# Kernel tuning notes

Measured on AMD Instinct MI355X. Metric: run time of the kernel, lower is better.

Reference implementation:

```python
import jax, jax.numpy as jnp
import numpy as np

DIM = 768
HEADS = 12
HEAD_DIM = DIM // HEADS
WS = 14  # window size
MLP = 3072
EPS = 1e-6
SCALE = HEAD_DIM ** -0.5
B, H, W = 4, 64, 64


def setup_inputs() -> dict:
    key = jax.random.key(0)
    ks = jax.random.split(key, 8)
    s = 0.02
    f32 = jnp.float32
    return {
        "hidden_states": jax.random.normal(ks[0], (B, DIM, H, W), f32),
        "ln1_w": jnp.ones((DIM,), f32),
        "ln1_b": jnp.zeros((DIM,), f32),
        "qkv_w": jax.random.normal(ks[1], (DIM, 3 * DIM), f32) * s,
        "qkv_b": jnp.zeros((3 * DIM,), f32),
        "proj_w": jax.random.normal(ks[2], (DIM, DIM), f32) * s,
        "proj_b": jnp.zeros((DIM,), f32),
        "rel_pos_h": jax.random.normal(ks[3], (2 * WS - 1, HEAD_DIM), f32) * s,
        "rel_pos_w": jax.random.normal(ks[4], (2 * WS - 1, HEAD_DIM), f32) * s,
        "ln2_w": jnp.ones((DIM,), f32),
        "ln2_b": jnp.zeros((DIM,), f32),
        "fc1_w": jax.random.normal(ks[5], (DIM, MLP), f32) * s,
        "fc1_b": jnp.zeros((MLP,), f32),
        "fc2_w": jax.random.normal(ks[6], (MLP, DIM), f32) * s,
        "fc2_b": jnp.zeros((DIM,), f32),
    }


def _layer_norm(x, w, b):
    mu = jnp.mean(x, axis=-1, keepdims=True)
    var = jnp.mean(jnp.square(x - mu), axis=-1, keepdims=True)
    return (x - mu) * jax.lax.rsqrt(var + EPS) * w + b


def _get_rel_pos(size, rel_pos):
    # q_size == k_size == WS, rel_pos already has 2*WS-1 rows -> pure gather
    coords = jnp.arange(size)[:, None] - jnp.arange(size)[None, :] + (size - 1)
    return rel_pos[coords]  # (size, size, head_dim)


def _attention(x, qkv_w, qkv_b, proj_w, proj_b, rel_pos_h, rel_pos_w):
    nb, h, w, c = x.shape  # windows batch, WS, WS, DIM
    n = h * w
    qkv = x.reshape(nb, n, c) @ qkv_w + qkv_b  # (nb, n, 3*DIM)
    qkv = qkv.reshape(nb, n, 3, HEADS, HEAD_DIM).transpose(2, 0, 3, 1, 4)
    qkv = qkv.reshape(3, nb * HEADS, n, HEAD_DIM)
    q, k, v = qkv[0], qkv[1], qkv[2]
    attn = jnp.einsum('bqc,bkc->bqk', q * SCALE, k)  # (nb*HEADS, n, n)
    # decomposed relative position bias
    Rh = _get_rel_pos(h, rel_pos_h)  # (h, h, hd)
    Rw = _get_rel_pos(w, rel_pos_w)  # (w, w, hd)
    rq = q.reshape(-1, h, w, HEAD_DIM)
    rel_h = jnp.einsum('bhwc,hkc->bhwk', rq, Rh)
    rel_w = jnp.einsum('bhwc,wkc->bhwk', rq, Rw)
    attn = (attn.reshape(-1, h, w, h, w)
            + rel_h[:, :, :, :, None]
            + rel_w[:, :, :, None, :]).reshape(-1, n, n)
    attn = jax.nn.softmax(attn, axis=-1)
    out = attn @ v  # (nb*HEADS, n, hd)
    out = out.reshape(nb, HEADS, h, w, HEAD_DIM).transpose(0, 2, 3, 1, 4)
    out = out.reshape(nb, h, w, c)
    return out @ proj_w + proj_b


def reference(hidden_states, ln1_w, ln1_b, qkv_w, qkv_b, proj_w, proj_b,
              rel_pos_h, rel_pos_w, ln2_w, ln2_b, fc1_w, fc1_b, fc2_w, fc2_b):
    x = hidden_states.transpose(0, 2, 3, 1)  # NCHW -> NHWC
    b, h, w, c = x.shape
    shortcut = x
    x = _layer_norm(x, ln1_w, ln1_b)
    # window partition with padding
    ph = (WS - h % WS) % WS
    pw = (WS - w % WS) % WS
    x = jnp.pad(x, ((0, 0), (0, ph), (0, pw), (0, 0)))
    hp, wp = h + ph, w + pw
    x = x.reshape(b, hp // WS, WS, wp // WS, WS, c).transpose(0, 1, 3, 2, 4, 5)
    windows = x.reshape(-1, WS, WS, c)
    windows = _attention(windows, qkv_w, qkv_b, proj_w, proj_b, rel_pos_h, rel_pos_w)
    # window unpartition + crop
    x = windows.reshape(b, hp // WS, wp // WS, WS, WS, c).transpose(0, 1, 3, 2, 4, 5)
    x = x.reshape(b, hp, wp, c)[:, :h, :w, :]
    x = shortcut + x
    y = _layer_norm(x, ln2_w, ln2_b)
    y = jax.nn.gelu(y @ fc1_w + fc1_b, approximate=False) @ fc2_w + fc2_b
    x = x + y
    return x.transpose(0, 3, 1, 2)  # back to NCHW
```

## Files before the change

### kernel.cpp

```cpp
#include <hip/hip_runtime.h>
#include <cstdint>
#include <cstddef>

#define NIMG   4
#define GRIDSZ 64
#define CH     768
#define NHEAD  12
#define WSZ    14
#define NWINS  100
#define NTOK   196
#define MWIN   19600
#define MREAL  16384
#define MLPC   3072
#define QKSCALE 0.125f

#define KSTR 72
#define VSTR 216
#define PSTR 40

typedef unsigned short u16;
typedef __attribute__((ext_vector_type(8))) short bf16x8;
typedef __attribute__((ext_vector_type(4))) float f32x4;

__device__ __forceinline__ float b2f(u16 u) {
  uint32_t x = (uint32_t)u << 16; float f; __builtin_memcpy(&f, &x, 4); return f;
}
__device__ __forceinline__ u16 f2b(float f) {
  uint32_t x; __builtin_memcpy(&x, &f, 4);
  x += 0x7fffu + ((x >> 16) & 1u);
  return (u16)(x >> 16);
}

__device__ __forceinline__ float fast_gelu(float x) {
  float z  = x * 0.70710678118654752440f;
  float az = fabsf(z);
  float t  = 1.0f / (1.0f + 0.3275911f * az);
  float poly = ((((1.061405429f * t - 1.453152027f) * t + 1.421413741f) * t
                 - 0.284496736f) * t + 0.254829592f) * t;
  float e  = __expf(-az * az);
  float erfv = copysignf(1.0f - poly * e, z);
  return 0.5f * x * (1.0f + erfv);
}

__device__ __forceinline__ void gl_lds16(const u16* g, u16* l) {
  __builtin_amdgcn_global_load_lds(
      (const __attribute__((address_space(1))) unsigned int*)g,
      (__attribute__((address_space(3))) unsigned int*)l, 16, 0, 0);
}

__global__ __launch_bounds__(256) void k_nchw2nhwc(const float* __restrict__ in,
                                                   float* __restrict__ out) {
  __shared__ float tile[32][33];
  int b  = blockIdx.z;
  int g0 = blockIdx.x * 32;
  int c0 = blockIdx.y * 32;
  int tx = threadIdx.x, ty = threadIdx.y;
  const float* ip = in + (size_t)b * CH * 4096;
  float* op = out + (size_t)b * 4096 * CH;
#pragma unroll
  for (int k = 0; k < 32; k += 8)
    tile[ty + k][tx] = ip[(size_t)(c0 + ty + k) * 4096 + g0 + tx];
  __syncthreads();
#pragma unroll
  for (int k = 0; k < 32; k += 8)
    op[(size_t)(g0 + ty + k) * CH + c0 + tx] = tile[tx][ty + k];
}

__global__ __launch_bounds__(256) void k_nhwc2nchw(const float* __restrict__ in,
                                                   float* __restrict__ out) {
  __shared__ float tile[32][33];
  int b  = blockIdx.z;
  int g0 = blockIdx.x * 32;
  int c0 = blockIdx.y * 32;
  int tx = threadIdx.x, ty = threadIdx.y;
  const float* ip = in + (size_t)b * 4096 * CH;
  float* op = out + (size_t)b * CH * 4096;
#pragma unroll
  for (int k = 0; k < 32; k += 8)
    tile[ty + k][tx] = ip[(size_t)(g0 + ty + k) * CH + c0 + tx];
  __syncthreads();
#pragma unroll
  for (int k = 0; k < 32; k += 8)
    op[(size_t)(c0 + ty + k) * 4096 + g0 + tx] = tile[tx][ty + k];
}

__global__ __launch_bounds__(256) void k_wt(const float* __restrict__ in,
                                            u16* __restrict__ out,
                                            int K, int N) {
  __shared__ float t[32][33];
  int n0 = blockIdx.x * 32, k0 = blockIdx.y * 32;
  int tx = threadIdx.x, ty = threadIdx.y;
#pragma unroll
  for (int k = 0; k < 32; k += 8)
    t[ty + k][tx] = in[(size_t)(k0 + ty + k) * N + n0 + tx];
  __syncthreads();
#pragma unroll
  for (int k = 0; k < 32; k += 8)
    out[(size_t)(n0 + ty + k) * K + k0 + tx] = f2b(t[tx][ty + k]);
}

__device__ __forceinline__ float block_sum(float s, float* red) {
  __syncthreads();
#pragma unroll
  for (int off = 32; off > 0; off >>= 1) s += __shfl_down(s, off, 64);
  int wid = threadIdx.x >> 6, lane = threadIdx.x & 63;
  if (lane == 0) red[wid] = s;
  __syncthreads();
  return red[0] + red[1] + red[2] + red[3];
}

__global__ __launch_bounds__(256) void k_ln(const float* __restrict__ x,
                                            const float* __restrict__ wt,
                                            const float* __restrict__ bs,
                                            u16* __restrict__ y,
                                            int window_mode) {
  __shared__ float red[4];
  int row = blockIdx.x, tid = threadIdx.x;
  const float* xp = x + (size_t)row * CH;
  float v0 = xp[tid], v1 = xp[tid + 256], v2 = xp[tid + 512];
  float mu = block_sum(v0 + v1 + v2, red) * (1.0f / 768.0f);
  float d0 = v0 - mu, d1 = v1 - mu, d2 = v2 - mu;
  float var = block_sum(d0 * d0 + d1 * d1 + d2 * d2, red) * (1.0f / 768.0f);
  float rs = rsqrtf(var + 1e-6f);
  int orow = row;
  if (window_mode) {
    int b = row >> 12, hw = row & 4095;
    int h = hw >> 6, wc = hw & 63;
    orow = (b * 25 + (h / WSZ) * 5 + (wc / WSZ)) * NTOK + (h % WSZ) * WSZ + (wc % WSZ);
  }
  u16* yp = y + (size_t)orow * CH;
  yp[tid]       = f2b(d0 * rs * wt[tid]       + bs[tid]);
  yp[tid + 256] = f2b(d1 * rs * wt[tid + 256] + bs[tid + 256]);
  yp[tid + 512] = f2b(d2 * rs * wt[tid + 512] + bs[tid + 512]);
}

__global__ __launch_bounds__(256, 3) void k_gemm_mfma(const u16* __restrict__ A,
                                                      const u16* __restrict__ BT,
                                                      const float* __restrict__ bias,
                                                      void* __restrict__ Cv,
                                                      u16* __restrict__ Vt,
                                                      int M, int N, int K,
                                                      int act, int mode, int row0) {
  __shared__ u16 As[3][128 * 32];
  __shared__ u16 Bs[3][128 * 32];
  int tid  = threadIdx.x;
  int lane = tid & 63, wave = tid >> 6;

  int gx   = gridDim.x, gy = gridDim.y;
  int nwg  = gx * gy;
  int orig = blockIdx.y * gx + blockIdx.x;
  int q = nwg >> 3, r = nwg & 7;
  int xcd = orig & 7, idx = orig >> 3;
  int wgid = (xcd < r ? xcd * (q + 1) : r * (q + 1) + (xcd - r) * q) + idx;

  int GM = 3145728 / (128 * K * 2);
  if (GM < 2) GM = 2;
  if (GM > gy) GM = gy;
  int gsz   = GM * gx;
  int grp   = wgid / gsz;
  int first = grp * GM;
  int gm    = gy - first; if (gm > GM) gm = GM;
  int loc   = wgid - grp * gsz;
  int bm    = first + loc % gm;
  int bn    = loc / gm;

  int wm = (wave & 1) * 64, wn = (wave >> 1) * 64;
  int l15 = lane & 15, quad = lane >> 4;
  int xq = (quad ^ ((l15 >> 1) & 3)) * 8;

  f32x4 acc[4][4];
#pragma unroll
  for (int i = 0; i < 4; i++)
#pragma unroll
    for (int j = 0; j < 4; j++) acc[i][j] = (f32x4){0.f, 0.f, 0.f, 0.f};

  const u16* Atile = A + (size_t)bm * 128 * K;
  const u16* Btile = BT + (size_t)bn * 128 * K;

  const u16* ga[2];
  const u16* gb[2];
#pragma unroll
  for (int i = 0; i < 2; ++i) {
    int c_ = i * 256 + wave * 64 + lane;
    int row_ = c_ >> 2, gs_ = (c_ & 3) ^ ((c_ >> 3) & 3);
    ga[i] = Atile + (size_t)row_ * K + gs_ * 8;
    gb[i] = Btile + (size_t)row_ * K + gs_ * 8;
  }

  const int nk = K >> 5;

#define STAGE(slot)                                                          \
  do {                                                                       \
    _Pragma("unroll")                                                        \
    for (int i = 0; i < 2; ++i) {                                            \
      gl_lds16(ga[i], &As[(slot)][(i * 256 + wave * 64) * 8]);               \
      ga[i] += 32;                                                           \
      gl_lds16(gb[i], &Bs[(slot)][(i * 256 + wave * 64) * 8]);               \
      gb[i] += 32;                                                           \
    }                                                                        \
  } while (0)

#define COMPUTE(slot)                                                        \
  do {                                                                       \
    bf16x8 af[4], bfv[4];                                                    \
    _Pragma("unroll")                                                        \
    for (int mi = 0; mi < 4; mi++)                                           \
      af[mi] = *(const bf16x8*)&As[(slot)][(wm + mi * 16 + l15) * 32 + xq];  \
    _Pragma("unroll")                                                        \
    for (int ni = 0; ni < 4; ni++)                                           \
      bfv[ni] = *(const bf16x8*)&Bs[(slot)][(wn + ni * 16 + l15) * 32 + xq]; \
    _Pragma("unroll")                                                        \
    for (int mi = 0; mi < 4; mi++)                                           \
      _Pragma("unroll")                                                      \
      for (int ni = 0; ni < 4; ni++)                                         \
        acc[mi][ni] = __builtin_amdgcn_mfma_f32_16x16x32_bf16(               \
            bfv[ni], af[mi], acc[mi][ni], 0, 0, 0);                          \
  } while (0)

#define WAITL                                                                \
  do {                                                                       \
    asm volatile("s_waitcnt vmcnt(4)" ::: "memory");                         \
    __builtin_amdgcn_s_barrier();                                            \
  } while (0)

  STAGE(0);
  STAGE(1);

  for (int g = 0; g < nk - 3; g += 3) {
    WAITL; STAGE(2); COMPUTE(0);
    WAITL; STAGE(0); COMPUTE(1);
    WAITL; STAGE(1); COMPUTE(2);
  }
  WAITL; STAGE(2); COMPUTE(0);
  WAITL;           COMPUTE(1);
  asm volatile("s_waitcnt vmcnt(0)" ::: "memory");
  __builtin_amdgcn_s_barrier();
  COMPUTE(2);

#undef STAGE
#undef COMPUTE
#undef WAITL

#pragma unroll
  for (int mi = 0; mi < 4; mi++) {
    int row = bm * 128 + wm + mi * 16 + l15;
    if (row >= M) continue;
    size_t gbase = 0;
    bool valid = true;
    int wloc = 0, tok = 0;
    if (mode == 2) {
      int rowa = row + row0;
      int widx = rowa / NTOK, tt = rowa % NTOK;
      int b = widx / 25, wq = widx % 25;
      int h = (wq / 5) * WSZ + tt / WSZ;
      int w = (wq % 5) * WSZ + tt % WSZ;
      valid = (h < GRIDSZ) && (w < GRIDSZ);
      gbase = valid ? ((size_t)((b * GRIDSZ + h) * GRIDSZ + w)) * CH : 0;
    }
    if (mode == 3) { wloc = row / NTOK; tok = row - wloc * NTOK; }
#pragma unroll
    for (int ni = 0; ni < 4; ni++) {
      int colb = bn * 128 + wn + ni * 16 + quad * 4;
      float4 b4 = *(const float4*)&bias[colb];
      float v[4] = {acc[mi][ni][0] + b4.x, acc[mi][ni][1] + b4.y,
                    acc[mi][ni][2] + b4.z, acc[mi][ni][3] + b4.w};
      if (act == 1) {
#pragma unroll
        for (int r2 = 0; r2 < 4; r2++) v[r2] = fast_gelu(v[r2]);
      }
      if (mode == 0) {
        ushort4 st = make_ushort4(f2b(v[0]), f2b(v[1]), f2b(v[2]), f2b(v[3]));
        *(ushort4*)((u16*)Cv + (size_t)row * N + colb) = st;
      } else if (mode == 1) {
        float4* p = (float4*)((float*)Cv + (size_t)row * N + colb);
        float4 o = *p;
        o.x += v[0]; o.y += v[1]; o.z += v[2]; o.w += v[3];
        *p = o;
      } else if (mode == 2) {
        if (valid) {
          float4* p = (float4*)((float*)Cv + gbase + colb);
          float4 o = *p;
          o.x += v[0]; o.y += v[1]; o.z += v[2]; o.w += v[3];
          *p = o;
        }
      } else {
        if (colb < 1536) {
          ushort4 st = make_ushort4(f2b(v[0]), f2b(v[1]), f2b(v[2]), f2b(v[3]));
          *(ushort4*)((u16*)Cv + (size_t)row * N + colb) = st;
        } else {
          int vv = colb - 1536, hd = vv >> 6, d = vv & 63;
          u16* vp = Vt + ((size_t)(wloc * NHEAD + hd) * 64 + d) * VSTR + tok;
#pragma unroll
          for (int r2 = 0; r2 < 4; r2++) vp[(size_t)r2 * VSTR] = f2b(v[r2]);
        }
      }
    }
  }
}

__global__ __launch_bounds__(256) void k_relbias(const u16* __restrict__ qkv,
                                                 const float* __restrict__ rel_h,
                                                 const float* __restrict__ rel_w,
                                                 u16* __restrict__ rhg,
                                                 u16* __restrict__ rwg,
                                                 int nrows) {
  int idx = blockIdx.x * 256 + threadIdx.x;
  if (idx >= nrows * NHEAD) return;
  int head = idx % NHEAD, row = idx / NHEAD;
  int wloc = row / NTOK, tok = row - wloc * NTOK;
  const u16* qp = qkv + (size_t)row * (3 * CH) + head * 64;
  float q[64];
#pragma unroll
  for (int d = 0; d < 64; d += 4) {
    ushort4 u4 = *(const ushort4*)(qp + d);
    q[d] = b2f(u4.x); q[d + 1] = b2f(u4.y); q[d + 2] = b2f(u4.z); q[d + 3] = b2f(u4.w);
  }
  int hq = tok / WSZ, wq = tok % WSZ;
  size_t obase = ((size_t)(wloc * NHEAD + head) * NTOK + tok) * 16;
  for (int kk = 0; kk < WSZ; kk++) {
    const float* rh = rel_h + (size_t)(hq - kk + WSZ - 1) * 64;
    const float* rw = rel_w + (size_t)(wq - kk + WSZ - 1) * 64;
    float sh = 0.0f, sw = 0.0f;
#pragma unroll
    for (int d = 0; d < 64; d++) { sh += q[d] * rh[d]; sw += q[d] * rw[d]; }
    rhg[obase + kk] = f2b(sh);
    rwg[obase + kk] = f2b(sw);
  }
}

__global__ __launch_bounds__(256) void k_attn_mfma(const u16* __restrict__ qkv,
                                                   const u16* __restrict__ Vt,
                                                   const u16* __restrict__ rhg,
                                                   const u16* __restrict__ rwg,
                                                   u16* __restrict__ out,
                                                   int win0) {
  __shared__ u16 Ks[NTOK * KSTR];
  __shared__ u16 Vs[64 * VSTR];
  __shared__ u16 Ps[4][16 * PSTR];
  int head = blockIdx.x, wloc = blockIdx.y;
  int tid = threadIdx.x, lane = tid & 63, wave = tid >> 6;
  int l15 = lane & 15, quad = lane >> 4;
  const u16* qbase = qkv + (size_t)wloc * NTOK * (3 * CH) + head * 64;

  for (int c = tid; c < NTOK * 8; c += 256) {
    int tok = c >> 3, part = c & 7;
    uint4 v = *(const uint4*)(qbase + (size_t)tok * (3 * CH) + CH + part * 8);
    *(uint4*)&Ks[tok * KSTR + part * 8] = v;
  }
  const u16* vb = Vt + (size_t)(wloc * NHEAD + head) * 64 * VSTR;
#pragma unroll
  for (int it = 0; it < 7; ++it) {
    int c = it * 256 + tid;
    if (c < 64 * VSTR / 8) gl_lds16(vb + (size_t)c * 8, Vs + ((size_t)it * 256 + wave * 64) * 8);
  }
  __syncthreads();

  const u16* rhp = rhg + ((size_t)(wloc * NHEAD + head) * NTOK) * 16;
  const u16* rwp = rwg + ((size_t)(wloc * NHEAD + head) * NTOK) * 16;
  int winabs = win0 + wloc;

  for (int t16 = wave; t16 < 13; t16 += 4) {
    int qtok = t16 * 16 + l15; if (qtok > NTOK - 1) qtok = NTOK - 1;
    bf16x8 aq0 = *(const bf16x8*)(qbase + (size_t)qtok * (3 * CH) + quad * 8);
    bf16x8 aq1 = *(const bf16x8*)(qbase + (size_t)qtok * (3 * CH) + 32 + quad * 8);

    f32x4 s[13];
#pragma unroll
    for (int ct = 0; ct < 13; ct++) s[ct] = (f32x4){0.f, 0.f, 0.f, 0.f};
#pragma unroll
    for (int ct = 0; ct < 13; ct++) {
      int ktok = ct * 16 + l15; if (ktok > NTOK - 1) ktok = NTOK - 1;
      bf16x8 bk0 = *(const bf16x8*)&Ks[ktok * KSTR + quad * 8];
      bf16x8 bk1 = *(const bf16x8*)&Ks[ktok * KSTR + 32 + quad * 8];
      s[ct] = __builtin_amdgcn_mfma_f32_16x16x32_bf16(aq0, bk0, s[ct], 0, 0, 0);
      s[ct] = __builtin_amdgcn_mfma_f32_16x16x32_bf16(aq1, bk1, s[ct], 0, 0, 0);
    }

    f32x4 o[4];
#pragma unroll
    for (int ni = 0; ni < 4; ni++) o[ni] = (f32x4){0.f, 0.f, 0.f, 0.f};
    float lsum[4] = {0.f, 0.f, 0.f, 0.f};
    int row0t = t16 * 16 + quad * 4;

#pragma unroll
    for (int cc = 0; cc < 7; ++cc) {
#pragma unroll
      for (int half = 0; half < 2; ++half) {
        int ct = cc * 2 + half;
        if (ct < 13) {
          int col = ct * 16 + l15;
          int jh = col / WSZ, jw = col - jh * WSZ;
          bool colok = col < NTOK;
#pragma unroll
          for (int r = 0; r < 4; r++) {
            int rowt = row0t + r; int rowc = rowt > NTOK - 1 ? NTOK - 1 : rowt;
            float bias = b2f(rhp[rowc * 16 + jh]) + b2f(rwp[rowc * 16 + jw]);
            float sv = s[ct][r] * QKSCALE + bias;
            float p = colok ? __expf(sv) : 0.f;
            lsum[r] += p;
            Ps[wave][(quad * 4 + r) * PSTR + half * 16 + l15] = f2b(p);
          }
        } else {
#pragma unroll
          for (int r = 0; r < 4; r++)
            Ps[wave][(quad * 4 + r) * PSTR + half * 16 + l15] = 0;
        }
      }
      bf16x8 pa = *(const bf16x8*)&Ps[wave][l15 * PSTR + quad * 8];
#pragma unroll
      for (int ni = 0; ni < 4; ni++) {
        bf16x8 bv = *(const bf16x8*)&Vs[(ni * 16 + l15) * VSTR + cc * 32 + quad * 8];
        o[ni] = __builtin_amdgcn_mfma_f32_16x16x32_bf16(pa, bv, o[ni], 0, 0, 0);
      }
    }

#pragma unroll
    for (int r = 0; r < 4; r++) {
#pragma unroll
      for (int m = 1; m < 16; m <<= 1) lsum[r] += __shfl_xor(lsum[r], m, 64);
    }

#pragma unroll
    for (int r = 0; r < 4; r++) {
      int rowt = row0t + r;
      if (rowt < NTOK) {
        float inv = 1.0f / lsum[r];
        u16* op = out + ((size_t)winabs * NTOK + rowt) * CH + head * 64;
#pragma unroll
        for (int ni = 0; ni < 4; ni++) op[ni * 16 + l15] = f2b(o[ni][r] * inv);
      }
    }
  }
}

extern "C" void kernel_launch(void* const* d_in, const int* in_sizes, int n_in,
                              void* d_out, int out_size, void* d_ws, size_t ws_size,
                              hipStream_t stream) {
  const float* hidden = (const float*)d_in[0];
  const float* ln1_w  = (const float*)d_in[1];
  const float* ln1_b  = (const float*)d_in[2];
  const float* qkv_w  = (const float*)d_in[3];
  const float* qkv_b  = (const float*)d_in[4];
  const float* proj_w = (const float*)d_in[5];
  const float* proj_b = (const float*)d_in[6];
  const float* rel_h  = (const float*)d_in[7];
  const float* rel_w  = (const float*)d_in[8];
  const float* ln2_w  = (const float*)d_in[9];
  const float* ln2_b  = (const float*)d_in[10];
  const float* fc1_w  = (const float*)d_in[11];
  const float* fc1_b  = (const float*)d_in[12];
  const float* fc2_w  = (const float*)d_in[13];
  const float* fc2_b  = (const float*)d_in[14];
  float* out = (float*)d_out;

  char* ws = (char*)d_ws;
  float* x_nhwc = (float*)ws;
  u16*   R1     = (u16*)(ws + 50331648);
  u16*   qkvT   = (u16*)(ws + 80437248);
  u16*   projT  = qkvT + (size_t)2304 * 768;
  u16*   fc1T   = projT + (size_t)768 * 768;
  u16*   fc2T   = fc1T + (size_t)3072 * 768;
  u16*   R2     = fc2T + (size_t)768 * 3072;
  size_t used   = (size_t)80437248 + 14155776;
  size_t r2e    = ws_size > used ? (ws_size - used) >> 1 : 0;

  const size_t PW_QKV = (size_t)NTOK * 3 * CH;
  const size_t PW_VT  = (size_t)NHEAD * 64 * VSTR;
  const size_t PW_RB  = (size_t)NHEAD * NTOK * 16;
  const size_t perwin = PW_QKV + PW_VT + 2 * PW_RB;
  size_t wc_s = r2e / perwin;
  int Wc = wc_s >= NWINS ? NWINS : (int)wc_s;
  if (Wc < 1) Wc = 1;
  size_t rc_s = (r2e / MLPC / 128) * 128;
  int Rc = rc_s >= MREAL ? MREAL : (int)rc_s;
  if (Rc < 128) Rc = 128;

  u16* Vt  = R2 + (size_t)Wc * PW_QKV;
  u16* rhg = Vt + (size_t)Wc * PW_VT;
  u16* rwg = rhg + (size_t)Wc * PW_RB;

  k_wt<<<dim3(72, 24), dim3(32, 8), 0, stream>>>(qkv_w, qkvT, CH, 3 * CH);
  k_wt<<<dim3(24, 24), dim3(32, 8), 0, stream>>>(proj_w, projT, CH, CH);
  k_wt<<<dim3(96, 24), dim3(32, 8), 0, stream>>>(fc1_w, fc1T, CH, MLPC);
  k_wt<<<dim3(24, 96), dim3(32, 8), 0, stream>>>(fc2_w, fc2T, MLPC, CH);

  hipMemsetAsync(R1, 0, (size_t)MWIN * CH * sizeof(u16), stream);

  k_nchw2nhwc<<<dim3(128, 24, NIMG), dim3(32, 8), 0, stream>>>(hidden, x_nhwc);
  k_ln<<<MREAL, 256, 0, stream>>>(x_nhwc, ln1_w, ln1_b, R1, 1);
  for (int w0 = 0; w0 < NWINS; w0 += Wc) {
    int wc = NWINS - w0 < Wc ? NWINS - w0 : Wc;
    int Mc = wc * NTOK;
    k_gemm_mfma<<<dim3(18, (Mc + 127) / 128), 256, 0, stream>>>(
        R1 + (size_t)w0 * NTOK * CH, qkvT, qkv_b, R2, Vt,
        Mc, 3 * CH, CH, 0, 3, 0);
    k_relbias<<<(Mc * NHEAD + 255) / 256, 256, 0, stream>>>(
        R2, rel_h, rel_w, rhg, rwg, Mc);
    k_attn_mfma<<<dim3(NHEAD, wc), 256, 0, stream>>>(
        R2, Vt, rhg, rwg, R1, w0);
  }
  k_gemm_mfma<<<dim3(6, (MWIN + 127) / 128), 256, 0, stream>>>(
      R1, projT, proj_b, x_nhwc, nullptr, MWIN, CH, CH, 0, 2, 0);
  k_ln<<<MREAL, 256, 0, stream>>>(x_nhwc, ln2_w, ln2_b, R1, 0);
  for (int r0 = 0; r0 < MREAL; r0 += Rc) {
    int rc = MREAL - r0 < Rc ? MREAL - r0 : Rc;
    k_gemm_mfma<<<dim3(24, (rc + 127) / 128), 256, 0, stream>>>(
        R1 + (size_t)r0 * CH, fc1T, fc1_b, R2, nullptr, rc, MLPC, CH, 1, 0, 0);
    k_gemm_mfma<<<dim3(6, (rc + 127) / 128), 256, 0, stream>>>(
        R2, fc2T, fc2_b, x_nhwc + (size_t)r0 * CH, nullptr, rc, CH, MLPC, 0, 1, 0);
  }
  k_nhwc2nchw<<<dim3(128, 24, NIMG), dim3(32, 8), 0, stream>>>(x_nhwc, out);
}
```

Measured before the change: 748.3 us.

## Add 256x256-tile 8-wave GEMM kernel for QKV and FC1 projections

```diff
diff --git a/kernel.cpp b/kernel.cpp
--- a/kernel.cpp
+++ b/kernel.cpp
@@ -134,6 +134,179 @@
   yp[tid + 512] = f2b(d2 * rs * wt[tid + 512] + bs[tid + 512]);
 }
 
+__device__ __forceinline__ void gemm_epilogue_row(
+    const f32x4* accrow, int row, int colbase, int N,
+    const float* __restrict__ bias, void* __restrict__ Cv,
+    u16* __restrict__ Vt, int act, int mode, int row0, int M) {
+  if (row >= M) return;
+  size_t gbase = 0;
+  bool valid = true;
+  int wloc = 0, tok = 0;
+  if (mode == 2) {
+    int rowa = row + row0;
+    int widx = rowa / NTOK, tt = rowa % NTOK;
+    int b = widx / 25, wq = widx % 25;
+    int h = (wq / 5) * WSZ + tt / WSZ;
+    int w = (wq % 5) * WSZ + tt % WSZ;
+    valid = (h < GRIDSZ) && (w < GRIDSZ);
+    gbase = valid ? ((size_t)((b * GRIDSZ + h) * GRIDSZ + w)) * CH : 0;
+  }
+  if (mode == 3) { wloc = row / NTOK; tok = row - wloc * NTOK; }
+#pragma unroll
+  for (int ni = 0; ni < 4; ni++) {
+    int colb = colbase + ni * 16;
+    float4 b4 = *(const float4*)&bias[colb];
+    float v[4] = {accrow[ni][0] + b4.x, accrow[ni][1] + b4.y,
+                  accrow[ni][2] + b4.z, accrow[ni][3] + b4.w};
+    if (act == 1) {
+#pragma unroll
+      for (int r2 = 0; r2 < 4; r2++) v[r2] = fast_gelu(v[r2]);
+    }
+    if (mode == 0) {
+      ushort4 st = make_ushort4(f2b(v[0]), f2b(v[1]), f2b(v[2]), f2b(v[3]));
+      *(ushort4*)((u16*)Cv + (size_t)row * N + colb) = st;
+    } else if (mode == 1) {
+      float4* p = (float4*)((float*)Cv + (size_t)row * N + colb);
+      float4 o = *p;
+      o.x += v[0]; o.y += v[1]; o.z += v[2]; o.w += v[3];
+      *p = o;
+    } else if (mode == 2) {
+      if (valid) {
+        float4* p = (float4*)((float*)Cv + gbase + colb);
+        float4 o = *p;
+        o.x += v[0]; o.y += v[1]; o.z += v[2]; o.w += v[3];
+        *p = o;
+      }
+    } else {
+      if (colb < 1536) {
+        ushort4 st = make_ushort4(f2b(v[0]), f2b(v[1]), f2b(v[2]), f2b(v[3]));
+        *(ushort4*)((u16*)Cv + (size_t)row * N + colb) = st;
+      } else {
+        int vv = colb - 1536, hd = vv >> 6, d = vv & 63;
+        u16* vp = Vt + ((size_t)(wloc * NHEAD + hd) * 64 + d) * VSTR + tok;
+#pragma unroll
+        for (int r2 = 0; r2 < 4; r2++) vp[(size_t)r2 * VSTR] = f2b(v[r2]);
+      }
+    }
+  }
+}
+
+__global__ __launch_bounds__(512, 1) void k_gemm8(const u16* __restrict__ A,
+                                                  const u16* __restrict__ BT,
+                                                  const float* __restrict__ bias,
+                                                  void* __restrict__ Cv,
+                                                  u16* __restrict__ Vt,
+                                                  int M, int N, int K,
+                                                  int act, int mode, int row0) {
+  __shared__ u16 As[3][256 * 32];
+  __shared__ u16 Bs[3][256 * 32];
+  int tid  = threadIdx.x;
+  int lane = tid & 63, wave = tid >> 6;
+
+  int gx = gridDim.x, gy = gridDim.y;
+  int nwg = gx * gy;
+  int orig = blockIdx.y * gx + blockIdx.x;
+  int q = nwg >> 3, r = nwg & 7;
+  int xcd = orig & 7, idx = orig >> 3;
+  int wgid = (xcd < r ? xcd * (q + 1) : r * (q + 1) + (xcd - r) * q) + idx;
+  int GM = 3145728 / (256 * K * 2);
+  if (GM < 2) GM = 2;
+  if (GM > gy) GM = gy;
+  int gsz = GM * gx;
+  int grp = wgid / gsz;
+  int first = grp * GM;
+  int gm = gy - first; if (gm > GM) gm = GM;
+  int loc = wgid - grp * gsz;
+  int bm = first + loc % gm;
+  int bn = loc / gm;
+
+  int wr = wave >> 2, wc = wave & 3;
+  int l15 = lane & 15, quad = lane >> 4;
+  int swz = (quad ^ ((l15 >> 1) & 3)) * 8;
+
+  f32x4 acc[8][4];
+#pragma unroll
+  for (int i = 0; i < 8; i++)
+#pragma unroll
+    for (int j = 0; j < 4; j++) acc[i][j] = (f32x4){0.f, 0.f, 0.f, 0.f};
+
+  const u16* Atile = A + (size_t)bm * 256 * K;
+  const u16* Btile = BT + (size_t)bn * 256 * K;
+
+  int rowc = tid >> 2;
+  int gsv  = ((tid & 3) ^ ((tid >> 3) & 3)) * 8;
+  const u16* pa = Atile + (size_t)rowc * K + gsv;
+  const u16* pb = Btile + (size_t)rowc * K + gsv;
+  int dstb = wave * 512;
+
+  int abase = (wr * 128 + l15) * 32 + swz;
+  int bbase = (wc * 64 + l15) * 32 + swz;
+
+  const int NT = K >> 5;
+
+#define STG_A(S2, T2, h) \
+  gl_lds16(pa + (size_t)(h) * 128 * K + (size_t)(T2) * 32, &As[(S2)][(h) * 4096 + dstb])
+#define STG_B(S2, T2, h) \
+  gl_lds16(pb + (size_t)(h) * 128 * K + (size_t)(T2) * 32, &Bs[(S2)][(h) * 4096 + dstb])
+
+#define GROUP(S, T)                                                          \
+  do {                                                                       \
+    if ((T) + 1 < NT) asm volatile("s_waitcnt vmcnt(4)" ::: "memory");       \
+    else              asm volatile("s_waitcnt vmcnt(0)" ::: "memory");       \
+    __builtin_amdgcn_s_barrier();                                            \
+    int T2_ = (T) + 2;                                                       \
+    bool st_ = T2_ < NT;                                                     \
+    bf16x8 bf_[4], af_[8];                                                   \
+    _Pragma("unroll")                                                        \
+    for (int ni = 0; ni < 4; ni++)                                           \
+      bf_[ni] = *(const bf16x8*)&Bs[(S)][bbase + ni * 512];                  \
+    _Pragma("unroll")                                                        \
+    for (int mi = 0; mi < 4; mi++)                                           \
+      af_[mi] = *(const bf16x8*)&As[(S)][abase + mi * 512];                  \
+    if (st_) { STG_A(((S) + 2) % 3, T2_, 0); STG_A(((S) + 2) % 3, T2_, 1); } \
+    _Pragma("unroll")                                                        \
+    for (int mi = 4; mi < 8; mi++)                                           \
+      af_[mi] = *(const bf16x8*)&As[(S)][abase + mi * 512];                  \
+    __builtin_amdgcn_s_setprio(1);                                           \
+    _Pragma("unroll")                                                        \
+    for (int mi = 0; mi < 4; mi++)                                           \
+      _Pragma("unroll")                                                      \
+      for (int ni = 0; ni < 4; ni++)                                         \
+        acc[mi][ni] = __builtin_amdgcn_mfma_f32_16x16x32_bf16(               \
+            bf_[ni], af_[mi], acc[mi][ni], 0, 0, 0);                         \
+    __builtin_amdgcn_s_setprio(0);                                           \
+    if (st_) { STG_B(((S) + 2) % 3, T2_, 0); STG_B(((S) + 2) % 3, T2_, 1); } \
+    __builtin_amdgcn_s_setprio(1);                                           \
+    _Pragma("unroll")                                                        \
+    for (int mi = 4; mi < 8; mi++)                                           \
+      _Pragma("unroll")                                                      \
+      for (int ni = 0; ni < 4; ni++)                                         \
+        acc[mi][ni] = __builtin_amdgcn_mfma_f32_16x16x32_bf16(               \
+            bf_[ni], af_[mi], acc[mi][ni], 0, 0, 0);                         \
+    __builtin_amdgcn_s_setprio(0);                                           \
+  } while (0)
+
+  STG_A(0, 0, 0); STG_A(0, 0, 1); STG_B(0, 0, 0); STG_B(0, 0, 1);
+  STG_A(1, 1, 0); STG_A(1, 1, 1); STG_B(1, 1, 0); STG_B(1, 1, 1);
+
+  for (int kt = 0; kt < NT; kt += 3) {
+    GROUP(0, kt);
+    GROUP(1, kt + 1);
+    GROUP(2, kt + 2);
+  }
+
+#undef GROUP
+#undef STG_A
+#undef STG_B
+
+#pragma unroll
+  for (int mi = 0; mi < 8; mi++) {
+    int row = bm * 256 + wr * 128 + mi * 16 + l15;
+    int colbase = bn * 256 + wc * 64 + quad * 4;
+    gemm_epilogue_row(acc[mi], row, colbase, N, bias, Cv, Vt, act, mode, row0, M);
+  }
+}
+
 __global__ __launch_bounds__(256, 3) void k_gemm_mfma(const u16* __restrict__ A,
                                                       const u16* __restrict__ BT,
                                                       const float* __restrict__ bias,
@@ -226,10 +399,12 @@
   STAGE(0);
   STAGE(1);
 
+  int t = 0;
   for (int g = 0; g < nk - 3; g += 3) {
     WAITL; STAGE(2); COMPUTE(0);
     WAITL; STAGE(0); COMPUTE(1);
     WAITL; STAGE(1); COMPUTE(2);
+    t += 3;
   }
   WAITL; STAGE(2); COMPUTE(0);
   WAITL;           COMPUTE(1);
@@ -244,57 +419,8 @@
 #pragma unroll
   for (int mi = 0; mi < 4; mi++) {
     int row = bm * 128 + wm + mi * 16 + l15;
-    if (row >= M) continue;
-    size_t gbase = 0;
-    bool valid = true;
-    int wloc = 0, tok = 0;
-    if (mode == 2) {
-      int rowa = row + row0;
-      int widx = rowa / NTOK, tt = rowa % NTOK;
-      int b = widx / 25, wq = widx % 25;
-      int h = (wq / 5) * WSZ + tt / WSZ;
-      int w = (wq % 5) * WSZ + tt % WSZ;
-      valid = (h < GRIDSZ) && (w < GRIDSZ);
-      gbase = valid ? ((size_t)((b * GRIDSZ + h) * GRIDSZ + w)) * CH : 0;
-    }
-    if (mode == 3) { wloc = row / NTOK; tok = row - wloc * NTOK; }
-#pragma unroll
-    for (int ni = 0; ni < 4; ni++) {
-      int colb = bn * 128 + wn + ni * 16 + quad * 4;
-      float4 b4 = *(const float4*)&bias[colb];
-      float v[4] = {acc[mi][ni][0] + b4.x, acc[mi][ni][1] + b4.y,
-                    acc[mi][ni][2] + b4.z, acc[mi][ni][3] + b4.w};
-      if (act == 1) {
-#pragma unroll
-        for (int r2 = 0; r2 < 4; r2++) v[r2] = fast_gelu(v[r2]);
-      }
-      if (mode == 0) {
-        ushort4 st = make_ushort4(f2b(v[0]), f2b(v[1]), f2b(v[2]), f2b(v[3]));
-        *(ushort4*)((u16*)Cv + (size_t)row * N + colb) = st;
-      } else if (mode == 1) {
-        float4* p = (float4*)((float*)Cv + (size_t)row * N + colb);
-        float4 o = *p;
-        o.x += v[0]; o.y += v[1]; o.z += v[2]; o.w += v[3];
-        *p = o;
-      } else if (mode == 2) {
-        if (valid) {
-          float4* p = (float4*)((float*)Cv + gbase + colb);
-          float4 o = *p;
-          o.x += v[0]; o.y += v[1]; o.z += v[2]; o.w += v[3];
-          *p = o;
-        }
-      } else {
-        if (colb < 1536) {
-          ushort4 st = make_ushort4(f2b(v[0]), f2b(v[1]), f2b(v[2]), f2b(v[3]));
-          *(ushort4*)((u16*)Cv + (size_t)row * N + colb) = st;
-        } else {
-          int vv = colb - 1536, hd = vv >> 6, d = vv & 63;
-          u16* vp = Vt + ((size_t)(wloc * NHEAD + hd) * 64 + d) * VSTR + tok;
-#pragma unroll
-          for (int r2 = 0; r2 < 4; r2++) vp[(size_t)r2 * VSTR] = f2b(v[r2]);
-        }
-      }
-    }
+    int colbase = bn * 128 + wn + quad * 4;
+    gemm_epilogue_row(acc[mi], row, colbase, N, bias, Cv, Vt, act, mode, row0, M);
   }
 }
 
@@ -471,9 +597,9 @@
   size_t wc_s = r2e / perwin;
   int Wc = wc_s >= NWINS ? NWINS : (int)wc_s;
   if (Wc < 1) Wc = 1;
-  size_t rc_s = (r2e / MLPC / 128) * 128;
+  size_t rc_s = (r2e / MLPC / 256) * 256;
   int Rc = rc_s >= MREAL ? MREAL : (int)rc_s;
-  if (Rc < 128) Rc = 128;
+  if (Rc < 256) Rc = 256;
 
   u16* Vt  = R2 + (size_t)Wc * PW_QKV;
   u16* rhg = Vt + (size_t)Wc * PW_VT;
@@ -491,7 +617,7 @@
   for (int w0 = 0; w0 < NWINS; w0 += Wc) {
     int wc = NWINS - w0 < Wc ? NWINS - w0 : Wc;
     int Mc = wc * NTOK;
-    k_gemm_mfma<<<dim3(18, (Mc + 127) / 128), 256, 0, stream>>>(
+    k_gemm8<<<dim3(9, (Mc + 255) / 256), 512, 0, stream>>>(
         R1 + (size_t)w0 * NTOK * CH, qkvT, qkv_b, R2, Vt,
         Mc, 3 * CH, CH, 0, 3, 0);
     k_relbias<<<(Mc * NHEAD + 255) / 256, 256, 0, stream>>>(
@@ -504,7 +630,7 @@
   k_ln<<<MREAL, 256, 0, stream>>>(x_nhwc, ln2_w, ln2_b, R1, 0);
   for (int r0 = 0; r0 < MREAL; r0 += Rc) {
     int rc = MREAL - r0 < Rc ? MREAL - r0 : Rc;
-    k_gemm_mfma<<<dim3(24, (rc + 127) / 128), 256, 0, stream>>>(
+    k_gemm8<<<dim3(12, (rc + 255) / 256), 512, 0, stream>>>(
         R1 + (size_t)r0 * CH, fc1T, fc1_b, R2, nullptr, rc, MLPC, CH, 1, 0, 0);
     k_gemm_mfma<<<dim3(6, (rc + 127) / 128), 256, 0, stream>>>(
         R2, fc2T, fc2_b, x_nhwc + (size_t)r0 * CH, nullptr, rc, CH, MLPC, 0, 1, 0);
```

Measured after the change: 849.4 us. 13.5% more time.
